# Performance work log

Hardware: AMD Instinct MI355X
Metric: run time of the kernel (lower is better)

Reference implementation:

```python
import jax, jax.numpy as jnp
import numpy as np

D = 256; NH = 8; HD = D // NH; L = 4; P = 4; NQ = 900; BS = 8; DFFN = 1024
SHAPES = np.array([[128, 128], [64, 64], [32, 32], [16, 16]])  # (H, W) per level, static metadata
NV = int((SHAPES[:, 0] * SHAPES[:, 1]).sum())
EPS = 1e-6


def setup_inputs():
    key = jax.random.key(0)
    ks = iter(jax.random.split(key, 48))

    def nrm(shape, scale=0.02):
        return jax.random.normal(next(ks), shape, jnp.float32) * scale

    lsi = np.concatenate([[0], np.cumsum(SHAPES[:, 0] * SHAPES[:, 1])[:-1]]).astype(np.int64)
    return {
        'tgt': nrm((NQ, BS, D), 1.0),
        'tgt_query_pos': nrm((NQ, BS, D), 1.0),
        'tgt_reference_points': jax.random.uniform(next(ks), (NQ, BS, L, 2), jnp.float32),
        'memory': nrm((NV, BS, D), 1.0),
        'memory_spatial_shapes': jnp.asarray(SHAPES, jnp.int32),
        'memory_level_start_index': jnp.asarray(lsi, jnp.int32),
        'w_norm_sa': jnp.ones((D,), jnp.float32),
        'w_norm_ca': jnp.ones((D,), jnp.float32),
        'w_norm_ffn': jnp.ones((D,), jnp.float32),
        'ls_sa': jnp.full((D,), 1e-4, jnp.float32),
        'ls_ca': jnp.full((D,), 1e-4, jnp.float32),
        'ls_ffn': jnp.full((D,), 1e-4, jnp.float32),
        'Wq': nrm((D, D)), 'Wk': nrm((D, D)), 'Wv': nrm((D, D)),
        'bq': jnp.zeros((D,), jnp.float32), 'bk': jnp.zeros((D,), jnp.float32), 'bv': jnp.zeros((D,), jnp.float32),
        'Wo_sa': nrm((D, D)), 'bo_sa': jnp.zeros((D,), jnp.float32),
        'Wv_proj': nrm((D, D)), 'bv_proj': jnp.zeros((D,), jnp.float32),
        'W_off': nrm((NH * L * P * 2, D)), 'b_off': nrm((NH * L * P * 2,), 0.1),
        'W_attn': nrm((NH * L * P, D)), 'b_attn': jnp.zeros((NH * L * P,), jnp.float32),
        'W_out_ca': nrm((D, D)), 'bo_ca': jnp.zeros((D,), jnp.float32),
        'Wg': nrm((DFFN, D)), 'bg': jnp.zeros((DFFN,), jnp.float32),
        'Wu': nrm((DFFN, D)), 'bu': jnp.zeros((DFFN,), jnp.float32),
        'Wf': nrm((D, DFFN)), 'bf': jnp.zeros((D,), jnp.float32),
    }


def rmsnorm(x, w):
    return x * jax.lax.rsqrt(jnp.mean(x * x, axis=-1, keepdims=True) + EPS) * w


def ms_deform_sample(v, loc, attw):
    # v: (bs, nv, NH, HD); loc: (bs, nq, NH, L, P, 2) normalized (x, y); attw: (bs, nq, NH, L, P)
    bs, nq = loc.shape[0], loc.shape[1]
    out = jnp.zeros((bs, nq, NH, HD), loc.dtype)
    b_idx = jnp.arange(bs)[:, None, None, None]
    h_idx = jnp.arange(NH)[None, None, :, None]
    start = 0
    for l in range(L):
        Hl, Wl = int(SHAPES[l, 0]), int(SHAPES[l, 1])
        vf = v[:, start:start + Hl * Wl]  # (bs, Hl*Wl, NH, HD)
        start += Hl * Wl
        # grid_sample(align_corners=False, padding=zeros) pixel mapping
        x = loc[:, :, :, l, :, 0] * Wl - 0.5
        y = loc[:, :, :, l, :, 1] * Hl - 0.5
        x0 = jnp.floor(x)
        y0 = jnp.floor(y)
        acc = jnp.zeros((bs, nq, NH, P, HD), loc.dtype)
        for dx in (0, 1):
            for dy in (0, 1):
                xi = x0 + dx
                yi = y0 + dy
                w = (1.0 - jnp.abs(x - xi)) * (1.0 - jnp.abs(y - yi))
                valid = (xi >= 0) & (xi <= Wl - 1) & (yi >= 0) & (yi <= Hl - 1)
                w = jnp.where(valid, w, 0.0)
                idx = (jnp.clip(yi, 0, Hl - 1) * Wl + jnp.clip(xi, 0, Wl - 1)).astype(jnp.int32)
                acc = acc + w[..., None] * vf[b_idx, idx, h_idx]  # (bs, nq, NH, P, HD)
        out = out + jnp.einsum('bqhp,bqhpd->bqhd', attw[:, :, :, l], acc)
    return out


def reference(tgt, tgt_query_pos, tgt_reference_points, memory, memory_spatial_shapes,
              memory_level_start_index, w_norm_sa, w_norm_ca, w_norm_ffn, ls_sa, ls_ca, ls_ffn,
              Wq, Wk, Wv, bq, bk, bv, Wo_sa, bo_sa, Wv_proj, bv_proj, W_off, b_off, W_attn,
              b_attn, W_out_ca, bo_ca, Wg, bg, Wu, bu, Wf, bf):
    nq, bs, d = tgt.shape
    # --- self-attention (pre-norm + LayerScale residual) ---
    xn = rmsnorm(tgt, w_norm_sa)
    qk = xn + tgt_query_pos
    q = (qk @ Wq.T + bq).reshape(nq, bs, NH, HD)
    k = (qk @ Wk.T + bk).reshape(nq, bs, NH, HD)
    vv = (xn @ Wv.T + bv).reshape(nq, bs, NH, HD)
    scores = jnp.einsum('qbhd,kbhd->bhqk', q, k) * (1.0 / np.sqrt(HD))
    attn = jax.nn.softmax(scores, axis=-1)
    sa = jnp.einsum('bhqk,kbhd->qbhd', attn, vv).reshape(nq, bs, d) @ Wo_sa.T + bo_sa
    tgt = tgt + ls_sa * sa
    # --- multi-scale deformable cross-attention (identity=zeros in original) ---
    xn = rmsnorm(tgt, w_norm_ca)
    qca = jnp.swapaxes(xn + tgt_query_pos, 0, 1)  # (bs, nq, d)
    val = (jnp.swapaxes(memory, 0, 1) @ Wv_proj.T + bv_proj).reshape(bs, -1, NH, HD)
    off = (qca @ W_off.T + b_off).reshape(bs, nq, NH, L, P, 2)
    attw = jax.nn.softmax((qca @ W_attn.T + b_attn).reshape(bs, nq, NH, L * P), axis=-1)
    attw = attw.reshape(bs, nq, NH, L, P)
    norm = jnp.asarray(SHAPES[:, ::-1].copy(), jnp.float32)  # (W, H) per level
    ref = jnp.swapaxes(tgt_reference_points, 0, 1)  # (bs, nq, L, 2)
    loc = ref[:, :, None, :, None, :] + off / norm[None, None, None, :, None, :]
    ca = ms_deform_sample(val, loc, attw).reshape(bs, nq, d) @ W_out_ca.T + bo_ca
    tgt = tgt + ls_ca * jnp.swapaxes(ca, 0, 1)
    # --- SwiGLU FFN ---
    xn = rmsnorm(tgt, w_norm_ffn)
    ffn = (jax.nn.silu(xn @ Wg.T + bg) * (xn @ Wu.T + bu)) @ Wf.T + bf
    return tgt + ls_ffn * ffn
```

## Files before the change

kernel.cpp:

```cpp
#include <hip/hip_runtime.h>

typedef unsigned short ushort_t;
typedef unsigned int uint32;
typedef __bf16 bf16x8 __attribute__((ext_vector_type(8)));
typedef float f32x4 __attribute__((ext_vector_type(4)));
typedef ushort_t us4 __attribute__((ext_vector_type(4)));

#define D_    256
#define NH_   8
#define HD_   32
#define NQ_   900
#define BS_   8
#define TOK_  7200
#define NV_   21760
#define QP_   928
#define DFFN_ 1024

__device__ __forceinline__ ushort_t f2bf(float x) {
    union { float f; uint32 u; } v; v.f = x;
    uint32 r = v.u + 0x7FFFu + ((v.u >> 16) & 1u);
    return (ushort_t)(r >> 16);
}
__device__ __forceinline__ float bf2f(ushort_t h) {
    union { uint32 u; float f; } v; v.u = ((uint32)h) << 16;
    return v.f;
}
__device__ __forceinline__ int imin(int a, int b) { return a < b ? a : b; }
__device__ __forceinline__ int imax(int a, int b) { return a > b ? a : b; }

__global__ __launch_bounds__(256) void cvtall_k(
    const float* __restrict__ s0, const float* __restrict__ s1, const float* __restrict__ s2,
    const float* __restrict__ s3, const float* __restrict__ s4, const float* __restrict__ s5,
    const float* __restrict__ s6, const float* __restrict__ s7, const float* __restrict__ s8,
    const float* __restrict__ s9, const float* __restrict__ s10, ushort_t* __restrict__ dst,
    const float* __restrict__ bq, const float* __restrict__ bk,
    const float* __restrict__ boff, const float* __restrict__ battn,
    float* __restrict__ bias_qk, float* __restrict__ bias_ol) {
    int tid = threadIdx.x;
    if (blockIdx.x == 0) {
        bias_qk[tid] = bq[tid];
        bias_qk[256 + tid] = bk[tid];
        bias_ol[tid] = boff[tid];
        if (tid < 128) bias_ol[256 + tid] = battn[tid];
    }
    int id = blockIdx.x * 256 + tid;
    const float* s; int off;
    if      (id <  16384) { s = s0;  off = id; }
    else if (id <  32768) { s = s1;  off = id - 16384; }
    else if (id <  49152) { s = s2;  off = id - 32768; }
    else if (id <  65536) { s = s3;  off = id - 49152; }
    else if (id <  81920) { s = s4;  off = id - 65536; }
    else if (id <  98304) { s = s5;  off = id - 81920; }
    else if (id < 114688) { s = s6;  off = id - 98304; }
    else if (id < 122880) { s = s7;  off = id - 114688; }
    else if (id < 188416) { s = s8;  off = id - 122880; }
    else if (id < 253952) { s = s9;  off = id - 188416; }
    else                  { s = s10; off = id - 253952; }
    f32x4 v = *(const f32x4*)(s + (size_t)off * 4);
    us4 t;
#pragma unroll
    for (int e = 0; e < 4; e++) t[e] = f2bf(v[e]);
    *(us4*)(dst + (size_t)id * 4) = t;
}

__global__ __launch_bounds__(256) void rms_k(const float* __restrict__ x,
                                             const float* __restrict__ pos,
                                             const float* __restrict__ wn,
                                             ushort_t* __restrict__ xn_out,
                                             ushort_t* __restrict__ qk_out) {
    int r = blockIdx.x, tid = threadIdx.x;
    float v = x[r * D_ + tid];
    float ss = v * v;
#pragma unroll
    for (int o = 32; o; o >>= 1) ss += __shfl_xor(ss, o, 64);
    __shared__ float part[4];
    if ((tid & 63) == 0) part[tid >> 6] = ss;
    __syncthreads();
    float tot = part[0] + part[1] + part[2] + part[3];
    float sc = rsqrtf(tot * (1.f / 256.f) + 1e-6f);
    float xn = v * sc * wn[tid];
    if (xn_out) xn_out[r * D_ + tid] = f2bf(xn);
    if (qk_out) qk_out[r * D_ + tid] = f2bf(xn + pos[r * D_ + tid]);
}

enum { EPI_RESID, EPI_QK2, EPI_VT, EPI_VAL, EPI_OFFLOG };

template <int EPI, bool AF32, int BM, int BN, int WGM, int WGN, int TK>
__global__ __launch_bounds__(WGM * WGN * 64) void gemm2_k(
    const void* __restrict__ Ap, const ushort_t* __restrict__ Wp,
    const float* __restrict__ bias, void* __restrict__ outp, void* __restrict__ outp2,
    int M, int N, int swz,
    const float* __restrict__ resid, const float* __restrict__ ls, float scale) {
    constexpr int THREADS = WGM * WGN * 64;
    constexpr int NK  = TK / 32;
    constexpr int LDK = 40;
    constexpr int WR  = BM / WGM, WC = BN / WGN;
    constexpr int FM  = WR / 16,  FN = WC / 16;
    constexpr int ACH = AF32 ? (BM * 32 / 4 / THREADS) : (BM * 32 / 8 / THREADS);
    constexpr int BCH = BN * 32 / 8 / THREADS;

    __shared__ __align__(16) ushort_t As[2][BM * LDK];
    __shared__ __align__(16) ushort_t Bs[2][BN * LDK];

    const int tid = threadIdx.x, l = tid & 63, w = tid >> 6;
    const int wm = w % WGM, wn = w / WGM;
    int by = blockIdx.y;
    if (swz) { int cpx = gridDim.y >> 3; by = (by & 7) * cpx + (by >> 3); }
    const int m0 = by * BM, n0 = blockIdx.x * BN;
    const int lr = l & 15, lkb = (l >> 4) * 8;

    const ushort_t* Ab = (const ushort_t*)Ap;
    const float*    Af = (const float*)Ap;

    int aRow[ACH], aK[ACH], bRow[BCH], bK[BCH];
#pragma unroll
    for (int ch = 0; ch < ACH; ch++) {
        int cid = ch * THREADS + tid;
        if constexpr (AF32) { aRow[ch] = cid >> 3; aK[ch] = (cid & 7) * 4; }
        else                { aRow[ch] = cid >> 2; aK[ch] = (cid & 3) * 8; }
    }
#pragma unroll
    for (int ch = 0; ch < BCH; ch++) {
        int cid = ch * THREADS + tid;
        bRow[ch] = cid >> 2; bK[ch] = (cid & 3) * 8;
    }
    int aGRow[ACH];
#pragma unroll
    for (int ch = 0; ch < ACH; ch++) aGRow[ch] = imin(m0 + aRow[ch], M - 1);

    f32x4  aSTf[AF32 ? ACH : 1];
    bf16x8 aSTb[AF32 ? 1 : ACH];
    bf16x8 bST[BCH];

    auto load_regs = [&](int kt) {
        const int k0 = kt * 32;
#pragma unroll
        for (int ch = 0; ch < ACH; ch++) {
            if constexpr (AF32)
                aSTf[ch] = *(const f32x4*)(Af + (size_t)aGRow[ch] * TK + k0 + aK[ch]);
            else
                aSTb[ch] = *(const bf16x8*)(Ab + (size_t)aGRow[ch] * TK + k0 + aK[ch]);
        }
#pragma unroll
        for (int ch = 0; ch < BCH; ch++)
            bST[ch] = *(const bf16x8*)(Wp + (size_t)(n0 + bRow[ch]) * TK + k0 + bK[ch]);
    };
    auto write_lds = [&](int buf) {
#pragma unroll
        for (int ch = 0; ch < ACH; ch++) {
            if constexpr (AF32) {
                us4 t;
#pragma unroll
                for (int e = 0; e < 4; e++) t[e] = f2bf(aSTf[ch][e]);
                *(us4*)&As[buf][aRow[ch] * LDK + aK[ch]] = t;
            } else {
                *(bf16x8*)&As[buf][aRow[ch] * LDK + aK[ch]] = aSTb[ch];
            }
        }
#pragma unroll
        for (int ch = 0; ch < BCH; ch++)
            *(bf16x8*)&Bs[buf][bRow[ch] * LDK + bK[ch]] = bST[ch];
    };

    f32x4 acc[FM][FN];
#pragma unroll
    for (int i = 0; i < FM; i++)
#pragma unroll
        for (int j = 0; j < FN; j++) acc[i][j] = f32x4{0.f, 0.f, 0.f, 0.f};

    load_regs(0);
    write_lds(0);
    __syncthreads();

    for (int kt = 0; kt < NK; ++kt) {
        const int c = kt & 1;
        if (kt + 1 < NK) load_regs(kt + 1);

        bf16x8 af[FM], bf_[FN];
#pragma unroll
        for (int i = 0; i < FM; i++)
            af[i] = *(const bf16x8*)&As[c][(wm * WR + i * 16 + lr) * LDK + lkb];
#pragma unroll
        for (int j = 0; j < FN; j++)
            bf_[j] = *(const bf16x8*)&Bs[c][(wn * WC + j * 16 + lr) * LDK + lkb];
#pragma unroll
        for (int i = 0; i < FM; i++)
#pragma unroll
            for (int j = 0; j < FN; j++)
                acc[i][j] = __builtin_amdgcn_mfma_f32_16x16x32_bf16(af[i], bf_[j], acc[i][j], 0, 0, 0);

        if (kt + 1 < NK) write_lds(c ^ 1);
        __syncthreads();
    }

#pragma unroll
    for (int i = 0; i < FM; i++)
#pragma unroll
        for (int j = 0; j < FN; j++) {
            int col = n0 + wn * WC + j * 16 + lr;
            float bvv = bias[col];
#pragma unroll
            for (int e = 0; e < 4; e++) {
                int row = m0 + wm * WR + i * 16 + (l >> 4) * 4 + e;
                if (row >= M) continue;
                float v = acc[i][j][e] + bvv;
                if constexpr (EPI == EPI_RESID) {
                    size_t idx = (size_t)row * N + col;
                    ((float*)outp)[idx] = resid[idx] + ls[col] * v;
                } else if constexpr (EPI == EPI_QK2) {
                    int c2 = col & 255;
                    int q = row >> 3, bb = row & 7, h = c2 >> 5, hd = c2 & 31;
                    ushort_t* dst = (col < 256) ? (ushort_t*)outp : (ushort_t*)outp2;
                    float sc = (col < 256) ? scale : 1.f;
                    dst[((bb * NH_ + h) * QP_ + q) * HD_ + hd] = f2bf(v * sc);
                } else if constexpr (EPI == EPI_VT) {
                    int q = row >> 3, bb = row & 7, h = col >> 5, hd = col & 31;
                    ((ushort_t*)outp)[((bb * NH_ + h) * HD_ + hd) * QP_ + q] = f2bf(v);
                } else if constexpr (EPI == EPI_VAL) {
                    int vv = row >> 3, bb = row & 7, h = col >> 5, d = col & 31;
                    ((ushort_t*)outp)[(((size_t)(bb * NH_ + h)) * NV_ + vv) * HD_ + d] = f2bf(v);
                } else if constexpr (EPI == EPI_OFFLOG) {
                    if (col < 256) ((float*)outp)[(size_t)row * 256 + col] = v;
                    else           ((float*)outp2)[(size_t)row * 128 + col - 256] = v;
                }
            }
        }
}

__global__ __launch_bounds__(512, 4) void gemm3_k(
    const float* __restrict__ Af, const ushort_t* __restrict__ Wp,
    const float* __restrict__ bias, ushort_t* __restrict__ outp, int swz) {
    constexpr int TK = 256, NK = 8;
    __shared__ __align__(16) ushort_t As[128 * 256];

    const int tid = threadIdx.x, l = tid & 63, w = tid >> 6;
    const int wm = w & 1, wn = w >> 1;
    int by = blockIdx.y;
    if (swz) { int cpx = gridDim.y >> 3; by = (by & 7) * cpx + (by >> 3); }
    const int m0 = by * 128;
    const int lr = l & 15, g = l >> 4;

#pragma unroll
    for (int ch = 0; ch < 8; ch++) {
        int c = ch * 512 + tid;
        int row = c >> 5, cg = c & 31;
        const f32x4* p = (const f32x4*)(Af + ((size_t)(m0 + row)) * TK + cg * 8);
        f32x4 p0 = p[0], p1 = p[1];
        bf16x8 t;
#pragma unroll
        for (int e = 0; e < 4; e++) { t[e] = (__bf16)p0[e]; t[4 + e] = (__bf16)p1[e]; }
        int cgs = cg ^ (row & 7);
        *(bf16x8*)&As[row * 256 + cgs * 8] = t;
    }
    __syncthreads();

    const int swzkey = lr & 7;
    const ushort_t* wBase = Wp + (size_t)(wn * 64 + lr) * TK + g * 8;

    f32x4 acc[4][4];
#pragma unroll
    for (int i = 0; i < 4; i++)
#pragma unroll
        for (int j = 0; j < 4; j++) acc[i][j] = f32x4{0.f, 0.f, 0.f, 0.f};

    bf16x8 bC[4], bN[4];
#pragma unroll
    for (int j = 0; j < 4; j++)
        bC[j] = *(const bf16x8*)(wBase + (size_t)j * 16 * TK);

    for (int kt = 0; kt < NK; ++kt) {
        if (kt + 1 < NK) {
#pragma unroll
            for (int j = 0; j < 4; j++)
                bN[j] = *(const bf16x8*)(wBase + (size_t)j * 16 * TK + (kt + 1) * 32);
        }
        bf16x8 af[4];
#pragma unroll
        for (int i = 0; i < 4; i++) {
            int row = wm * 64 + i * 16 + lr;
            int cg = (kt * 4 + g) ^ swzkey;
            af[i] = *(const bf16x8*)&As[row * 256 + cg * 8];
        }
#pragma unroll
        for (int i = 0; i < 4; i++)
#pragma unroll
            for (int j = 0; j < 4; j++)
                acc[i][j] = __builtin_amdgcn_mfma_f32_16x16x32_bf16(af[i], bC[j], acc[i][j], 0, 0, 0);
#pragma unroll
        for (int j = 0; j < 4; j++) bC[j] = bN[j];
    }

#pragma unroll
    for (int i = 0; i < 4; i++)
#pragma unroll
        for (int j = 0; j < 4; j++) {
            int col = wn * 64 + j * 16 + lr;
            float bvv = bias[col];
            int h = col >> 5, d = col & 31;
#pragma unroll
            for (int e = 0; e < 4; e++) {
                int row = m0 + wm * 64 + i * 16 + g * 4 + e;
                int vv = row >> 3, bb = row & 7;
                float v = acc[i][j][e] + bvv;
                outp[(((size_t)(bb * NH_ + h)) * NV_ + vv) * HD_ + d] = f2bf(v);
            }
        }
}

__global__ __launch_bounds__(256) void ffn_k(
    const ushort_t* __restrict__ Ap, const ushort_t* __restrict__ Wg,
    const ushort_t* __restrict__ Wu, const float* __restrict__ bgp,
    const float* __restrict__ bup, ushort_t* __restrict__ outp, int M) {
    constexpr int BM = 64, BN = 128, TK = 256, NK = TK / 32, LDK = 40;
    constexpr int WR = 32, WC = 64, FM = 2, FN = 4;

    __shared__ __align__(16) ushort_t As[2][BM * LDK];
    __shared__ __align__(16) ushort_t Gs[2][BN * LDK];
    __shared__ __align__(16) ushort_t Us[2][BN * LDK];

    const int tid = threadIdx.x, l = tid & 63, w = tid >> 6;
    const int wm = w & 1, wn = w >> 1;
    const int m0 = blockIdx.y * BM, n0 = blockIdx.x * BN;
    const int lr = l & 15, lkb = (l >> 4) * 8;

    const int aRow = tid >> 2, aK = (tid & 3) * 8;
    int bRow[2], bK[2];
#pragma unroll
    for (int ch = 0; ch < 2; ch++) { int cid = ch * 256 + tid; bRow[ch] = cid >> 2; bK[ch] = (cid & 3) * 8; }
    const int aGRow = imin(m0 + aRow, M - 1);

    bf16x8 aST, gST[2], uST[2];
    auto load_regs = [&](int kt) {
        const int k0 = kt * 32;
        aST = *(const bf16x8*)(Ap + (size_t)aGRow * TK + k0 + aK);
#pragma unroll
        for (int ch = 0; ch < 2; ch++) {
            gST[ch] = *(const bf16x8*)(Wg + (size_t)(n0 + bRow[ch]) * TK + k0 + bK[ch]);
            uST[ch] = *(const bf16x8*)(Wu + (size_t)(n0 + bRow[ch]) * TK + k0 + bK[ch]);
        }
    };
    auto write_lds = [&](int buf) {
        *(bf16x8*)&As[buf][aRow * LDK + aK] = aST;
#pragma unroll
        for (int ch = 0; ch < 2; ch++) {
            *(bf16x8*)&Gs[buf][bRow[ch] * LDK + bK[ch]] = gST[ch];
            *(bf16x8*)&Us[buf][bRow[ch] * LDK + bK[ch]] = uST[ch];
        }
    };

    f32x4 accG[FM][FN], accU[FM][FN];
#pragma unroll
    for (int i = 0; i < FM; i++)
#pragma unroll
        for (int j = 0; j < FN; j++) { accG[i][j] = f32x4{0,0,0,0}; accU[i][j] = f32x4{0,0,0,0}; }

    load_regs(0);
    write_lds(0);
    __syncthreads();

    for (int kt = 0; kt < NK; ++kt) {
        const int c = kt & 1;
        if (kt + 1 < NK) load_regs(kt + 1);
        bf16x8 af[FM], gf[FN], uf[FN];
#pragma unroll
        for (int i = 0; i < FM; i++)
            af[i] = *(const bf16x8*)&As[c][(wm * WR + i * 16 + lr) * LDK + lkb];
#pragma unroll
        for (int j = 0; j < FN; j++) {
            gf[j] = *(const bf16x8*)&Gs[c][(wn * WC + j * 16 + lr) * LDK + lkb];
            uf[j] = *(const bf16x8*)&Us[c][(wn * WC + j * 16 + lr) * LDK + lkb];
        }
#pragma unroll
        for (int i = 0; i < FM; i++)
#pragma unroll
            for (int j = 0; j < FN; j++) {
                accG[i][j] = __builtin_amdgcn_mfma_f32_16x16x32_bf16(af[i], gf[j], accG[i][j], 0, 0, 0);
                accU[i][j] = __builtin_amdgcn_mfma_f32_16x16x32_bf16(af[i], uf[j], accU[i][j], 0, 0, 0);
            }
        if (kt + 1 < NK) write_lds(c ^ 1);
        __syncthreads();
    }

#pragma unroll
    for (int i = 0; i < FM; i++)
#pragma unroll
        for (int j = 0; j < FN; j++) {
            int col = n0 + wn * WC + j * 16 + lr;
            float bg_ = bgp[col], bu_ = bup[col];
#pragma unroll
            for (int e = 0; e < 4; e++) {
                int row = m0 + wm * WR + i * 16 + (l >> 4) * 4 + e;
                if (row >= M) continue;
                float g = accG[i][j][e] + bg_;
                float u = accU[i][j][e] + bu_;
                float s = g / (1.f + __expf(-g));
                outp[(size_t)row * DFFN_ + col] = f2bf(s * u);
            }
        }
}

__global__ __launch_bounds__(256) void attn2_k(const ushort_t* __restrict__ qb,
                                               const ushort_t* __restrict__ kb,
                                               const ushort_t* __restrict__ vtb,
                                               ushort_t* __restrict__ sab) {
    __shared__ __align__(16) ushort_t Pl[4][16 * 40];
    const int tid = threadIdx.x, l = tid & 63, w = tid >> 6;
    const int bh = blockIdx.y, b = bh >> 3, h = bh & 7;
    const int q0 = (blockIdx.x * 4 + w) * 16;
    if (q0 >= NQ_) return;
    const int q = l & 15, g = l >> 4;
    ushort_t* Pw = &Pl[w][0];

    const bf16x8 qf = *(const bf16x8*)(qb + ((size_t)bh * QP_ + q0 + q) * HD_ + g * 8);
    const ushort_t* kbase = kb + (size_t)bh * QP_ * HD_;
    const ushort_t* vbase = vtb + (size_t)bh * HD_ * QP_;

    f32x4 O0 = {0.f, 0.f, 0.f, 0.f}, O1 = {0.f, 0.f, 0.f, 0.f};
    float m = -1e30f, sl = 0.f;

    auto ldk = [&](int t, int u) {
        return *(const bf16x8*)(kbase + (size_t)(t * 32 + u * 16 + q) * HD_ + g * 8);
    };
    auto ldv = [&](int t, int dh) {
        return *(const bf16x8*)(vbase + (size_t)(dh * 16 + q) * QP_ + t * 32 + g * 8);
    };
    bf16x8 kA = ldk(0, 0), kB = ldk(0, 1), v0 = ldv(0, 0), v1 = ldv(0, 1);

    for (int t = 0; t < 29; ++t) {
        bf16x8 nkA, nkB, nv0, nv1;
        if (t < 28) { nkA = ldk(t + 1, 0); nkB = ldk(t + 1, 1); nv0 = ldv(t + 1, 0); nv1 = ldv(t + 1, 1); }
        const f32x4 z = {0.f, 0.f, 0.f, 0.f};
        f32x4 sA = __builtin_amdgcn_mfma_f32_16x16x32_bf16(kA, qf, z, 0, 0, 0);
        f32x4 sB = __builtin_amdgcn_mfma_f32_16x16x32_bf16(kB, qf, z, 0, 0, 0);
        if (t == 28) {
            int k0 = 896 + g * 4;
#pragma unroll
            for (int e = 0; e < 4; e++) {
                if (k0 + e >= NQ_)      sA[e] = -1e30f;
                if (k0 + 16 + e >= NQ_) sB[e] = -1e30f;
            }
        }
        float tm = fmaxf(fmaxf(fmaxf(sA[0], sA[1]), fmaxf(sA[2], sA[3])),
                         fmaxf(fmaxf(sB[0], sB[1]), fmaxf(sB[2], sB[3])));
        tm = fmaxf(tm, __shfl_xor(tm, 16, 64));
        tm = fmaxf(tm, __shfl_xor(tm, 32, 64));
        float mn = fmaxf(m, tm);
        float r = exp2f(m - mn);
        m = mn;
#pragma unroll
        for (int e = 0; e < 4; e++) { O0[e] *= r; O1[e] *= r; }
        float pA[4], pB[4], ps = 0.f;
#pragma unroll
        for (int e = 0; e < 4; e++) {
            pA[e] = exp2f(sA[e] - m); pB[e] = exp2f(sB[e] - m);
            ps += pA[e] + pB[e];
        }
        sl = sl * r + ps;
        uint32 a0, a1, b0, b1;
        asm("v_cvt_pk_bf16_f32 %0, %1, %2" : "=v"(a0) : "v"(pA[0]), "v"(pA[1]));
        asm("v_cvt_pk_bf16_f32 %0, %1, %2" : "=v"(a1) : "v"(pA[2]), "v"(pA[3]));
        asm("v_cvt_pk_bf16_f32 %0, %1, %2" : "=v"(b0) : "v"(pB[0]), "v"(pB[1]));
        asm("v_cvt_pk_bf16_f32 %0, %1, %2" : "=v"(b1) : "v"(pB[2]), "v"(pB[3]));
        { uint2 tt; tt.x = a0; tt.y = a1; *(uint2*)(Pw + q * 40 + g * 4) = tt; }
        { uint2 tt; tt.x = b0; tt.y = b1; *(uint2*)(Pw + q * 40 + 16 + g * 4) = tt; }
        bf16x8 pf = *(const bf16x8*)(Pw + q * 40 + g * 8);
        O0 = __builtin_amdgcn_mfma_f32_16x16x32_bf16(v0, pf, O0, 0, 0, 0);
        O1 = __builtin_amdgcn_mfma_f32_16x16x32_bf16(v1, pf, O1, 0, 0, 0);
        kA = nkA; kB = nkB; v0 = nv0; v1 = nv1;
    }

    sl += __shfl_xor(sl, 16, 64);
    sl += __shfl_xor(sl, 32, 64);
    float inv = 1.f / sl;
    int row_q = q0 + q;
    if (row_q < NQ_) {
        ushort_t* op = sab + ((size_t)row_q * BS_ + b) * D_ + h * HD_ + g * 4;
#pragma unroll
        for (int dh = 0; dh < 2; dh++) {
            f32x4 Ov = dh ? O1 : O0;
            float e0 = Ov[0] * inv, e1 = Ov[1] * inv, e2 = Ov[2] * inv, e3 = Ov[3] * inv;
            uint32 w0, w1;
            asm("v_cvt_pk_bf16_f32 %0, %1, %2" : "=v"(w0) : "v"(e0), "v"(e1));
            asm("v_cvt_pk_bf16_f32 %0, %1, %2" : "=v"(w1) : "v"(e2), "v"(e3));
            *(uint32*)(op + dh * 16) = w0;
            *(uint32*)(op + dh * 16 + 2) = w1;
        }
    }
}

__global__ __launch_bounds__(256) void deform_k(
    const float* __restrict__ offb, const float* __restrict__ logb,
    const float* __restrict__ refpts, const int* __restrict__ shapes,
    const int* __restrict__ lsi, const ushort_t* __restrict__ val,
    ushort_t* __restrict__ ca) {
    __shared__ float off_l[256];
    __shared__ float attw[128];
    const int r = blockIdx.x;
    const int b = r & 7;
    const int tid = threadIdx.x;

    off_l[tid] = offb[(size_t)r * 256 + tid];
    if (tid < 128) {
        float lg = logb[(size_t)r * 128 + tid];
        float m = lg;
#pragma unroll
        for (int o = 1; o < 16; o <<= 1) m = fmaxf(m, __shfl_xor(m, o, 16));
        float e = __expf(lg - m);
        float s = e;
#pragma unroll
        for (int o = 1; o < 16; o <<= 1) s += __shfl_xor(s, o, 16);
        attw[tid] = e / s;
    }
    __syncthreads();

    const int h = tid >> 5, d = tid & 31;
    const ushort_t* vb = val + ((size_t)(b * NH_ + h)) * NV_ * HD_;
    float acc = 0.f;
#pragma unroll
    for (int lvl = 0; lvl < 4; lvl++) {
        const int H = shapes[lvl * 2], W = shapes[lvl * 2 + 1];
        const int base = lsi[lvl];
        const float refx = refpts[(r * 4 + lvl) * 2];
        const float refy = refpts[(r * 4 + lvl) * 2 + 1];
#pragma unroll
        for (int p = 0; p < 4; p++) {
            int oi = ((h * 4 + lvl) * 4 + p) * 2;
            float x = (refx + off_l[oi] / (float)W) * (float)W - 0.5f;
            float y = (refy + off_l[oi + 1] / (float)H) * (float)H - 0.5f;
            float x0 = floorf(x), y0 = floorf(y);
            float fx = x - x0, fy = y - y0;
            int ix = (int)x0, iy = (int)y0;
            float sval = 0.f;
#pragma unroll
            for (int dy = 0; dy <= 1; dy++)
#pragma unroll
                for (int dx = 0; dx <= 1; dx++) {
                    int xi = ix + dx, yi = iy + dy;
                    float wq = (dx ? fx : 1.f - fx) * (dy ? fy : 1.f - fy);
                    if (xi < 0 || xi >= W || yi < 0 || yi >= H) wq = 0.f;
                    int cx = imin(imax(xi, 0), W - 1), cy = imin(imax(yi, 0), H - 1);
                    float vv = bf2f(vb[(size_t)(base + cy * W + cx) * HD_ + d]);
                    sval += wq * vv;
                }
            acc += attw[h * 16 + lvl * 4 + p] * sval;
        }
    }
    ca[(size_t)r * 256 + tid] = f2bf(acc);
}

extern "C" void kernel_launch(void* const* d_in, const int* in_sizes, int n_in,
                              void* d_out, int out_size, void* d_ws, size_t ws_size,
                              hipStream_t stream) {
    (void)in_sizes; (void)n_in; (void)out_size; (void)ws_size;
    const float* tgt    = (const float*)d_in[0];
    const float* qpos   = (const float*)d_in[1];
    const float* refp   = (const float*)d_in[2];
    const float* mem    = (const float*)d_in[3];
    const int*   shapes = (const int*)d_in[4];
    const int*   lsi    = (const int*)d_in[5];
    const float* wnsa   = (const float*)d_in[6];
    const float* wnca   = (const float*)d_in[7];
    const float* wnffn  = (const float*)d_in[8];
    const float* lssa   = (const float*)d_in[9];
    const float* lsca   = (const float*)d_in[10];
    const float* lsffn  = (const float*)d_in[11];
    const float* Wq = (const float*)d_in[12];
    const float* Wk = (const float*)d_in[13];
    const float* Wv = (const float*)d_in[14];
    const float* bq = (const float*)d_in[15];
    const float* bk = (const float*)d_in[16];
    const float* bvv = (const float*)d_in[17];
    const float* Wo_sa = (const float*)d_in[18];
    const float* bo_sa = (const float*)d_in[19];
    const float* Wv_proj = (const float*)d_in[20];
    const float* bv_proj = (const float*)d_in[21];
    const float* W_off = (const float*)d_in[22];
    const float* b_off = (const float*)d_in[23];
    const float* W_attn = (const float*)d_in[24];
    const float* b_attn = (const float*)d_in[25];
    const float* W_out = (const float*)d_in[26];
    const float* bo_ca = (const float*)d_in[27];
    const float* Wg = (const float*)d_in[28];
    const float* bg = (const float*)d_in[29];
    const float* Wu = (const float*)d_in[30];
    const float* bu = (const float*)d_in[31];
    const float* Wf = (const float*)d_in[32];
    const float* bff = (const float*)d_in[33];

    char* ws = (char*)d_ws;
    size_t o = 0;
    auto alloc = [&](size_t b) { size_t c = o; o += (b + 255) & ~(size_t)255; return c; };

    const size_t wq_o = alloc(65536 * 2), wk_o = alloc(65536 * 2), wv_o = alloc(65536 * 2);
    const size_t wosa_o = alloc(65536 * 2), wvp_o = alloc(65536 * 2), wout_o = alloc(65536 * 2);
    const size_t woff_o = alloc(65536 * 2), wattn_o = alloc(32768 * 2);
    const size_t wg_o = alloc(262144 * 2), wu_o = alloc(262144 * 2), wf_o = alloc(262144 * 2);
    const size_t bqk_o = alloc(512 * 4), bol_o = alloc(384 * 4);
    const size_t xnsa_o = alloc((size_t)TOK_ * D_ * 2);
    const size_t qksa_o = alloc((size_t)TOK_ * D_ * 2);
    const size_t qkvBytes = (size_t)BS_ * NH_ * QP_ * HD_ * 2;
    const size_t qb_o = alloc(qkvBytes);
    const size_t kb_o = alloc(qkvBytes);
    const size_t vt_o = alloc(qkvBytes + 512);
    const size_t sa_o = alloc((size_t)TOK_ * D_ * 2);
    const size_t tgt1_o = alloc((size_t)TOK_ * D_ * 4);
    const size_t qca_o = alloc((size_t)TOK_ * D_ * 2);
    const size_t offb_o = alloc((size_t)TOK_ * 256 * 4);
    const size_t logit_o = alloc((size_t)TOK_ * 128 * 4);
    const size_t ca_o = alloc((size_t)TOK_ * D_ * 2);
    const size_t tgt2_o = alloc((size_t)TOK_ * D_ * 4);
    const size_t val_o = alloc((size_t)NV_ * BS_ * D_ * 2);
    const size_t h_o  = val_o;
    const size_t xn3_o = h_o + (size_t)TOK_ * DFFN_ * 2;

    dim3 blk(256);
    cvtall_k<<<dim3(319488 / 256), blk, 0, stream>>>(
        Wq, Wk, Wv, Wo_sa, Wv_proj, W_out, W_off, W_attn, Wg, Wu, Wf,
        (ushort_t*)(ws + wq_o),
        bq, bk, b_off, b_attn, (float*)(ws + bqk_o), (float*)(ws + bol_o));

    (void)hipMemsetAsync(ws + vt_o, 0, qkvBytes + 512, stream);

    rms_k<<<dim3(TOK_), blk, 0, stream>>>(tgt, qpos, wnsa,
                                          (ushort_t*)(ws + xnsa_o), (ushort_t*)(ws + qksa_o));
    const float QSC = 0.25503321550239915f;
    gemm2_k<EPI_QK2, false, 64, 128, 2, 2, 256><<<dim3(4, 113), blk, 0, stream>>>(
        ws + qksa_o, (ushort_t*)(ws + wq_o), (const float*)(ws + bqk_o),
        ws + qb_o, ws + kb_o, TOK_, 512, 0, nullptr, nullptr, QSC);
    gemm2_k<EPI_VT, false, 64, 128, 2, 2, 256><<<dim3(2, 113), blk, 0, stream>>>(
        ws + xnsa_o, (ushort_t*)(ws + wv_o), bvv, ws + vt_o, nullptr, TOK_, 256, 0,
        nullptr, nullptr, 1.f);
    attn2_k<<<dim3(15, 64), blk, 0, stream>>>((ushort_t*)(ws + qb_o), (ushort_t*)(ws + kb_o),
                                              (ushort_t*)(ws + vt_o), (ushort_t*)(ws + sa_o));
    gemm2_k<EPI_RESID, false, 64, 128, 2, 2, 256><<<dim3(2, 113), blk, 0, stream>>>(
        ws + sa_o, (ushort_t*)(ws + wosa_o), bo_sa, ws + tgt1_o, nullptr, TOK_, 256, 0,
        tgt, lssa, 1.f);

    rms_k<<<dim3(TOK_), blk, 0, stream>>>((const float*)(ws + tgt1_o), qpos, wnca,
                                          nullptr, (ushort_t*)(ws + qca_o));
    gemm2_k<EPI_OFFLOG, false, 64, 128, 2, 2, 256><<<dim3(3, 113), blk, 0, stream>>>(
        ws + qca_o, (ushort_t*)(ws + woff_o), (const float*)(ws + bol_o),
        ws + offb_o, ws + logit_o, TOK_, 384, 0, nullptr, nullptr, 1.f);
    gemm3_k<<<dim3(1, 1360), dim3(512), 0, stream>>>(
        mem, (ushort_t*)(ws + wvp_o), bv_proj, (ushort_t*)(ws + val_o), 1);
    deform_k<<<dim3(TOK_), blk, 0, stream>>>(
        (const float*)(ws + offb_o), (const float*)(ws + logit_o), refp, shapes, lsi,
        (ushort_t*)(ws + val_o), (ushort_t*)(ws + ca_o));
    gemm2_k<EPI_RESID, false, 64, 128, 2, 2, 256><<<dim3(2, 113), blk, 0, stream>>>(
        ws + ca_o, (ushort_t*)(ws + wout_o), bo_ca, ws + tgt2_o, nullptr, TOK_, 256, 0,
        (const float*)(ws + tgt1_o), lsca, 1.f);

    rms_k<<<dim3(TOK_), blk, 0, stream>>>((const float*)(ws + tgt2_o), nullptr, wnffn,
                                          (ushort_t*)(ws + xn3_o), nullptr);
    ffn_k<<<dim3(8, 113), blk, 0, stream>>>(
        (const ushort_t*)(ws + xn3_o), (const ushort_t*)(ws + wg_o),
        (const ushort_t*)(ws + wu_o), bg, bu, (ushort_t*)(ws + h_o), TOK_);
    gemm2_k<EPI_RESID, false, 64, 128, 2, 2, 1024><<<dim3(2, 113), blk, 0, stream>>>(
        ws + h_o, (ushort_t*)(ws + wf_o), bff, d_out, nullptr, TOK_, 256, 0,
        (const float*)(ws + tgt2_o), lsffn, 1.f);
}
```

Before: 368.9 us.

## Stage value-projection output in LDS for coalesced head-major stores; drop B prefetch

The value-projection GEMM epilogue now writes bias-added bf16 results into the shared A tile, then each thread copies contiguous 32-element head rows to the (batch, head, value, dim) output with 16-byte vector stores. Previously each lane did scattered 2-byte stores into the permuted layout. The register double-buffering of B fragments is also removed, so B is loaded each k-step. This saves registers but exposes global load latency, and it adds two barriers.

```diff
diff --git a/kernel.cpp b/kernel.cpp
--- a/kernel.cpp
+++ b/kernel.cpp
@@ -263,18 +263,11 @@
 #pragma unroll
         for (int j = 0; j < 4; j++) acc[i][j] = f32x4{0.f, 0.f, 0.f, 0.f};
 
-    bf16x8 bC[4], bN[4];
-#pragma unroll
-    for (int j = 0; j < 4; j++)
-        bC[j] = *(const bf16x8*)(wBase + (size_t)j * 16 * TK);
-
     for (int kt = 0; kt < NK; ++kt) {
-        if (kt + 1 < NK) {
-#pragma unroll
-            for (int j = 0; j < 4; j++)
-                bN[j] = *(const bf16x8*)(wBase + (size_t)j * 16 * TK + (kt + 1) * 32);
-        }
-        bf16x8 af[4];
+        bf16x8 bC[4], af[4];
+#pragma unroll
+        for (int j = 0; j < 4; j++)
+            bC[j] = *(const bf16x8*)(wBase + (size_t)j * 16 * TK + kt * 32);
 #pragma unroll
         for (int i = 0; i < 4; i++) {
             int row = wm * 64 + i * 16 + lr;
@@ -286,25 +279,42 @@
 #pragma unroll
             for (int j = 0; j < 4; j++)
                 acc[i][j] = __builtin_amdgcn_mfma_f32_16x16x32_bf16(af[i], bC[j], acc[i][j], 0, 0, 0);
-#pragma unroll
-        for (int j = 0; j < 4; j++) bC[j] = bN[j];
-    }
-
+    }
+
+    __syncthreads();
 #pragma unroll
     for (int i = 0; i < 4; i++)
 #pragma unroll
         for (int j = 0; j < 4; j++) {
             int col = wn * 64 + j * 16 + lr;
             float bvv = bias[col];
-            int h = col >> 5, d = col & 31;
 #pragma unroll
             for (int e = 0; e < 4; e++) {
-                int row = m0 + wm * 64 + i * 16 + g * 4 + e;
-                int vv = row >> 3, bb = row & 7;
-                float v = acc[i][j][e] + bvv;
-                outp[(((size_t)(bb * NH_ + h)) * NV_ + vv) * HD_ + d] = f2bf(v);
+                int row = wm * 64 + i * 16 + g * 4 + e;
+                As[row * 256 + col] = f2bf(acc[i][j][e] + bvv);
             }
         }
+    __syncthreads();
+    {
+        const int chunk = tid >> 3, sub = tid & 7;
+        const int bb = chunk >> 3, hh = chunk & 7;
+        const int vv0 = (m0 >> 3) + sub * 2;
+        ushort_t* obase = outp + (((size_t)(bb * NH_ + hh)) * NV_ + vv0) * HD_;
+#pragma unroll
+        for (int r2 = 0; r2 < 2; r2++) {
+            int lrow = (sub * 2 + r2) * 8 + bb;
+            const ushort_t* src = &As[lrow * 256 + hh * 32];
+            bf16x8 t0 = *(const bf16x8*)(src);
+            bf16x8 t1 = *(const bf16x8*)(src + 8);
+            bf16x8 t2 = *(const bf16x8*)(src + 16);
+            bf16x8 t3 = *(const bf16x8*)(src + 24);
+            ushort_t* dst = obase + r2 * HD_;
+            *(bf16x8*)(dst)      = t0;
+            *(bf16x8*)(dst + 8)  = t1;
+            *(bf16x8*)(dst + 16) = t2;
+            *(bf16x8*)(dst + 24) = t3;
+        }
+    }
 }
 
 __global__ __launch_bounds__(256) void ffn_k(
```

New measurement: 374.0 us. Within noise of the previous version (+1.4%).
